# Kernel tuning notes

Measured on AMD Instinct MI355X. Metric: run time of the kernel, lower is better.

The kernel has to match this reference:

```python
import jax, jax.numpy as jnp
from jax import lax
import numpy as np

T, B, S, H = 64, 512, 10, 1024

def setup_inputs() -> dict:
    key = jax.random.key(0)
    ks = jax.random.split(key, 5)
    sc_in = 1.0 / np.sqrt(S)
    sc_h = 1.0 / np.sqrt(H)
    return {
        "inputs": jax.random.normal(ks[0], (T, B, S), jnp.float32),
        "W_in": jax.random.normal(ks[1], (S, H), jnp.float32) * sc_in,
        "b_in": jnp.zeros((H,), jnp.float32),
        "W_ih": jax.random.normal(ks[2], (4 * H, H), jnp.float32) * sc_h,
        "W_hh": jax.random.normal(ks[3], (4 * H, H), jnp.float32) * sc_h,
        "b_ih": jnp.zeros((4 * H,), jnp.float32),
        "b_hh": jnp.zeros((4 * H,), jnp.float32),
        "W_out": jax.random.normal(ks[4], (H, S), jnp.float32) * sc_h,
        "b_out": jnp.zeros((S,), jnp.float32),
    }

def reference(inputs, W_in, b_in, W_ih, W_hh, b_ih, b_hh, W_out, b_out):
    # inputs: [T, B, S]
    t, b, s = inputs.shape
    h_dim = W_hh.shape[1]
    # input Linear: S -> H, for all timesteps at once
    x = inputs @ W_in + b_in                               # [T, B, H]
    # precompute input contribution to LSTM gates (PyTorch gate order i,f,g,o)
    xg = jnp.einsum('tbh,gh->tbg', x, W_ih) + (b_ih + b_hh)  # [T, B, 4H]

    def cell(carry, xg_t):
        h, c = carry
        gates = xg_t + h @ W_hh.T                          # [B, 4H]
        i, f, g, o = jnp.split(gates, 4, axis=-1)
        i = jax.nn.sigmoid(i)
        f = jax.nn.sigmoid(f)
        g = jnp.tanh(g)
        o = jax.nn.sigmoid(o)
        c = f * c + i * g
        h = o * jnp.tanh(c)
        return (h, c), h

    h0 = jnp.zeros((b, h_dim), inputs.dtype)
    _, hs = lax.scan(cell, (h0, h0), xg)                   # hs: [T, B, H]
    out = hs @ W_out + b_out                               # [T, B, S]
    return jnp.transpose(out, (1, 0, 2))                   # [B, T, S] (stack dim=1)
```

## Files before the change

kernel.cpp:

```cpp
#include <hip/hip_runtime.h>
#include <hip/hip_bf16.h>
#include <stdint.h>

#define T_STEPS 64
#define BATCH   512
#define SDIM    10
#define HDIM    1024
#define GDIM    4096

typedef __attribute__((ext_vector_type(8))) short bf16x8;
typedef __attribute__((ext_vector_type(4))) float f32x4;

#define MFMA16(a,b,c) __builtin_amdgcn_mfma_f32_16x16x32_bf16(a,b,c,0,0,0)
#define VMW(N) asm volatile("s_waitcnt vmcnt(" #N ")" ::: "memory")
#define LGKM0  asm volatile("s_waitcnt lgkmcnt(0)" ::: "memory")
#define SBAR   do { __builtin_amdgcn_s_barrier(); __builtin_amdgcn_sched_barrier(0); } while (0)

__device__ __forceinline__ float sigmoidf_(float x) { return 1.0f / (1.0f + __expf(-x)); }
__device__ __forceinline__ float tanhf_(float x) {
    x = fminf(15.0f, fmaxf(-15.0f, x));
    float e = __expf(2.0f * x);
    return (e - 1.0f) / (e + 1.0f);
}
__device__ __forceinline__ short bf16bits(float v) {
    __hip_bfloat16 hb = __float2bfloat16(v);
    return *(short*)&hb;
}

__device__ __forceinline__ void gload16(const void* g, void* l) {
    __builtin_amdgcn_global_load_lds(
        (const __attribute__((address_space(1))) unsigned int*)g,
        (__attribute__((address_space(3))) unsigned int*)l, 16, 0, 0);
}

__global__ void setup_kernel(const float* __restrict__ W_hh,
                             const float* __restrict__ W_out,
                             __hip_bfloat16* __restrict__ whh_bf,
                             __hip_bfloat16* __restrict__ wot_bf) {
    int idx = blockIdx.x * blockDim.x + threadIdx.x;
    int stride = gridDim.x * blockDim.x;
    for (int i = idx; i < GDIM * HDIM; i += stride)
        whh_bf[i] = __float2bfloat16(W_hh[i]);
    for (int i = idx; i < 16 * HDIM; i += stride) {
        int n = i >> 10, k = i & 1023;
        wot_bf[i] = (n < SDIM) ? __float2bfloat16(W_out[k * SDIM + n]) : __float2bfloat16(0.0f);
    }
}

__launch_bounds__(256)
__global__ void weq_kernel(const float* __restrict__ W_in,
                           const float* __restrict__ W_ih,
                           const float* __restrict__ b_in,
                           const float* __restrict__ b_ih,
                           const float* __restrict__ b_hh,
                           __hip_bfloat16* __restrict__ weq_bf) {
    __shared__ float sWin[SDIM * HDIM];
    __shared__ float sbin[HDIM];
    const int tid = threadIdx.x;
    for (int i = tid; i < SDIM * HDIM; i += 256) sWin[i] = W_in[i];
    for (int i = tid; i < HDIM; i += 256) sbin[i] = b_in[i];
    __syncthreads();
    const int wv = tid >> 6, lane = tid & 63;
#pragma unroll
    for (int j = 0; j < 4; ++j) {
        int n = blockIdx.x * 16 + wv * 4 + j;
        float acc[SDIM + 1];
#pragma unroll
        for (int s = 0; s <= SDIM; s++) acc[s] = 0.0f;
        for (int it = 0; it < HDIM / 64; ++it) {
            int k = lane + it * 64;
            float wih = W_ih[n * HDIM + k];
#pragma unroll
            for (int s = 0; s < SDIM; s++) acc[s] += wih * sWin[s * HDIM + k];
            acc[SDIM] += wih * sbin[k];
        }
#pragma unroll
        for (int s = 0; s <= SDIM; s++) {
            float v = acc[s];
            for (int off = 32; off > 0; off >>= 1) v += __shfl_down(v, off);
            acc[s] = v;
        }
        if (lane == 0) {
            __hip_bfloat16 rowv[32];
#pragma unroll
            for (int s = 0; s < SDIM; s++) rowv[s] = __float2bfloat16(acc[s]);
            rowv[10] = __float2bfloat16(acc[SDIM] + b_ih[n] + b_hh[n]);
#pragma unroll
            for (int s = 11; s < 32; s++) rowv[s] = __float2bfloat16(0.0f);
#pragma unroll
            for (int q = 0; q < 4; q++)
                ((uint4*)(weq_bf + n * 32))[q] = ((uint4*)rowv)[q];
        }
    }
}

__launch_bounds__(256)
__global__ void t0_kernel(const float* __restrict__ inputs,
                          const __hip_bfloat16* __restrict__ weq_bf,
                          __hip_bfloat16* __restrict__ hs,
                          float* __restrict__ c_buf) {
    int gidx = blockIdx.x * 256 + threadIdx.x;
    int b = gidx >> 10, h = gidx & 1023;
    float xv[SDIM];
#pragma unroll
    for (int s = 0; s < SDIM; s++) xv[s] = inputs[b * SDIM + s];
    float pre[4];
#pragma unroll
    for (int g = 0; g < 4; ++g) {
        const __hip_bfloat16* wr = weq_bf + (size_t)(g * HDIM + h) * 32;
        float a = __bfloat162float(wr[10]);
#pragma unroll
        for (int s = 0; s < SDIM; s++) a += xv[s] * __bfloat162float(wr[s]);
        pre[g] = a;
    }
    float ig = sigmoidf_(pre[0]);
    float gg = tanhf_(pre[2]);
    float og = sigmoidf_(pre[3]);
    float cn = ig * gg;
    c_buf[gidx] = cn;
    hs[gidx] = __float2bfloat16(og * tanhf_(cn));
}

__launch_bounds__(256, 1)
__global__ void step_kernel(const float* __restrict__ inputs,
                            const __hip_bfloat16* __restrict__ weq_bf,
                            const __hip_bfloat16* __restrict__ whh,
                            __hip_bfloat16* __restrict__ hs,
                            float* __restrict__ c_buf,
                            int t) {
    __shared__ __align__(16) unsigned char lds[122880];
    unsigned char* augA = lds + 98304;
    unsigned char* augB = lds + 106496;

    const int tid = threadIdx.x;
    const int wv = tid >> 6, lane = tid & 63;
    const int wm = wv >> 1, wn = wv & 1;
    const int lr = lane & 15, lk = lane >> 4;

    const int bid = blockIdx.x;
    const int nb = (bid & 7) * 4 + ((bid >> 3) & 3);
    const int mb = bid >> 5;
    const int m0 = mb * 64, h0 = nb * 32;

    const __hip_bfloat16* hprev = hs + (size_t)(t - 1) * BATCH * HDIM;

    const int srow = lane >> 3, sc8 = lane & 7;
    const __hip_bfloat16* aSrc[2]; int aDst[2];
#pragma unroll
    for (int j = 0; j < 2; j++) {
        int row = wv * 16 + j * 8 + srow;
        aSrc[j] = hprev + (size_t)(m0 + row) * HDIM + ((sc8 ^ (row & 7)) << 3);
        aDst[j] = wv * 2048 + j * 1024;
    }
    const __hip_bfloat16* bSrc[4]; int bDst[4];
#pragma unroll
    for (int j = 0; j < 4; j++) {
        int c = wv * 32 + j * 8 + srow;
        int n = (c & 3) * HDIM + h0 + (c >> 2);
        bSrc[j] = whh + (size_t)n * HDIM + ((sc8 ^ (c & 7)) << 3);
        bDst[j] = 8192 + wv * 4096 + j * 1024;
    }

    auto STAGE = [&](int kt) {
        const int base = (kt & 3) * 24576;
        const int ko = kt * 64;
        gload16(aSrc[0] + ko, lds + base + aDst[0]);
        gload16(aSrc[1] + ko, lds + base + aDst[1]);
        gload16(bSrc[0] + ko, lds + base + bDst[0]);
        gload16(bSrc[1] + ko, lds + base + bDst[1]);
        gload16(bSrc[2] + ko, lds + base + bDst[2]);
        gload16(bSrc[3] + ko, lds + base + bDst[3]);
    };

    *(uint4*)(augA + tid * 32) = (uint4){0, 0, 0, 0};
    *(uint4*)(augA + tid * 32 + 16) = (uint4){0, 0, 0, 0};

    float4 xv4 = {0.f, 0.f, 0.f, 0.f};
    if (tid < 160) xv4 = *(const float4*)(inputs + (size_t)(t * BATCH + m0) * SDIM + tid * 4);
    uint4 wb[2];
#pragma unroll
    for (int i = 0; i < 2; i++) {
        int q = tid + i * 256, c = q >> 2, ch = q & 3;
        int n = (c & 3) * HDIM + h0 + (c >> 2);
        wb[i] = *(const uint4*)(weq_bf + (size_t)n * 32 + ch * 8);
    }

    STAGE(0); STAGE(1); STAGE(2);

    LGKM0; SBAR;

    if (tid < 160) {
        float xf[4] = {xv4.x, xv4.y, xv4.z, xv4.w};
#pragma unroll
        for (int q = 0; q < 4; q++) {
            int idx = tid * 4 + q, row = idx / SDIM, col = idx - row * SDIM;
            *(short*)(augA + ((row * 128 + col * 2) ^ ((row & 7) << 4))) = bf16bits(xf[q]);
        }
    }
    if (tid < 64)
        *(short*)(augA + ((tid * 128 + 20) ^ ((tid & 7) << 4))) = (short)0x3F80;
#pragma unroll
    for (int i = 0; i < 2; i++) {
        int q = tid + i * 256, c = q >> 2, ch = q & 3;
        *(uint4*)(augB + c * 128 + ((ch * 16) ^ ((c & 7) << 4))) = wb[i];
    }
    LGKM0; SBAR;

    int aro[2], asz[2], bro[4], bsz[4];
#pragma unroll
    for (int fm = 0; fm < 2; fm++) {
        int row = wm * 32 + fm * 16 + lr;
        aro[fm] = row * 128; asz[fm] = (row & 7) << 4;
    }
#pragma unroll
    for (int fn = 0; fn < 4; fn++) {
        int c = wn * 64 + fn * 16 + lr;
        bro[fn] = c * 128; bsz[fn] = (c & 7) << 4;
    }

    f32x4 acc[2][4];
#pragma unroll
    for (int fm = 0; fm < 2; fm++)
#pragma unroll
        for (int fn = 0; fn < 4; fn++) {
            f32x4 z = {0.f, 0.f, 0.f, 0.f};
            acc[fm][fn] = z;
        }
    {
        bf16x8 a[2], b[4];
#pragma unroll
        for (int fm = 0; fm < 2; fm++)
            a[fm] = *(const bf16x8*)(augA + aro[fm] + ((lk * 16) ^ asz[fm]));
#pragma unroll
        for (int fn = 0; fn < 4; fn++)
            b[fn] = *(const bf16x8*)(augB + bro[fn] + ((lk * 16) ^ bsz[fn]));
#pragma unroll
        for (int fm = 0; fm < 2; fm++)
#pragma unroll
            for (int fn = 0; fn < 4; fn++)
                acc[fm][fn] = MFMA16(a[fm], b[fn], acc[fm][fn]);
    }

    for (int i = 0; i < 16; ++i) {
        if (i < 14)      { VMW(12); }
        else if (i == 14){ VMW(6);  }
        else             { VMW(0);  }
        SBAR;
        if (i < 13) STAGE(i + 3);
        const unsigned char* Ab = lds + (i & 3) * 24576;
        const unsigned char* Bb = Ab + 8192;
#pragma unroll
        for (int ks = 0; ks < 2; ++ks) {
            const int lo = ks * 64 + lk * 16;
            bf16x8 a[2], b[4];
#pragma unroll
            for (int fm = 0; fm < 2; fm++)
                a[fm] = *(const bf16x8*)(Ab + aro[fm] + (lo ^ asz[fm]));
#pragma unroll
            for (int fn = 0; fn < 4; fn++)
                b[fn] = *(const bf16x8*)(Bb + bro[fn] + (lo ^ bsz[fn]));
#pragma unroll
            for (int fm = 0; fm < 2; fm++)
#pragma unroll
                for (int fn = 0; fn < 4; fn++)
                    acc[fm][fn] = MFMA16(a[fm], b[fn], acc[fm][fn]);
        }
    }

#pragma unroll
    for (int fm = 0; fm < 2; fm++)
#pragma unroll
        for (int fn = 0; fn < 4; fn++)
#pragma unroll
            for (int r = 0; r < 4; r++) {
                int row = wm * 32 + fm * 16 + lk * 4 + r;
                int col = wn * 64 + fn * 16 + lr;
                *(float*)(lds + ((row * 512 + col * 4) ^ ((row & 7) << 4))) = acc[fm][fn][r];
            }
    LGKM0; SBAR;

    {
        const int row = tid >> 2, hh0 = (tid & 3) * 8;
        const size_t gbase = (size_t)(m0 + row) * HDIM + h0 + hh0;
        float4 c0 = *(float4*)(c_buf + gbase);
        float4 c1 = *(float4*)(c_buf + gbase + 4);
        float cold[8] = {c0.x, c0.y, c0.z, c0.w, c1.x, c1.y, c1.z, c1.w};
        float cnew[8];
        short hv[8];
#pragma unroll
        for (int j = 0; j < 8; j++) {
            float4 g4 = *(const float4*)(lds + ((row * 512 + (hh0 + j) * 16) ^ ((row & 7) << 4)));
            float ig = sigmoidf_(g4.x);
            float fg = sigmoidf_(g4.y);
            float gg = tanhf_(g4.z);
            float og = sigmoidf_(g4.w);
            float cn = fg * cold[j] + ig * gg;
            cnew[j] = cn;
            hv[j] = bf16bits(og * tanhf_(cn));
        }
        *(float4*)(c_buf + gbase) = (float4){cnew[0], cnew[1], cnew[2], cnew[3]};
        *(float4*)(c_buf + gbase + 4) = (float4){cnew[4], cnew[5], cnew[6], cnew[7]};
        *(uint4*)(hs + (size_t)t * BATCH * HDIM + gbase) = *(uint4*)hv;
    }
}

__launch_bounds__(256)
__global__ void out_mfma(const __hip_bfloat16* __restrict__ hs,
                         const __hip_bfloat16* __restrict__ wot,
                         const float* __restrict__ b_out,
                         float* __restrict__ out) {
    __shared__ __align__(16) unsigned char sW[32768];
    const int tid = threadIdx.x, lane = tid & 63, wv = tid >> 6;
    const int lr = lane & 15, lk = lane >> 4;
#pragma unroll
    for (int i = 0; i < 8; i++) {
        int q = tid + i * 256;
        int row = q >> 7, col = q & 127;
        uint4 v = *(const uint4*)(wot + row * 1024 + col * 8);
        *(uint4*)(sW + row * 2048 + ((col * 16) ^ ((row & 7) << 4))) = v;
    }
    float bo = (lr < SDIM) ? b_out[lr] : 0.0f;
    __syncthreads();
    const int sw = (lr & 7) << 4;
    const int brow = lr * 2048;
#pragma unroll
    for (int s2 = 0; s2 < 2; s2++) {
        int strip = blockIdx.x * 8 + wv * 2 + s2;
        const __hip_bfloat16* Ab = hs + (size_t)(strip * 16 + lr) * 1024 + lk * 8;
        f32x4 acc = {0.f, 0.f, 0.f, 0.f};
        for (int kc = 0; kc < 32; kc++) {
            bf16x8 a = *(const bf16x8*)(Ab + kc * 32);
            bf16x8 b = *(const bf16x8*)(sW + brow + ((kc * 64 + lk * 16) ^ sw));
            acc = MFMA16(a, b, acc);
        }
        if (lr < SDIM) {
#pragma unroll
            for (int r = 0; r < 4; r++) {
                int grow = strip * 16 + lk * 4 + r;
                out[(grow & 511) * (T_STEPS * SDIM) + (grow >> 9) * SDIM + lr] = acc[r] + bo;
            }
        }
    }
}

extern "C" void kernel_launch(void* const* d_in, const int* in_sizes, int n_in,
                              void* d_out, int out_size, void* d_ws, size_t ws_size,
                              hipStream_t stream) {
    const float* inputs = (const float*)d_in[0];
    const float* W_in   = (const float*)d_in[1];
    const float* b_in   = (const float*)d_in[2];
    const float* W_ih   = (const float*)d_in[3];
    const float* W_hh   = (const float*)d_in[4];
    const float* b_ih   = (const float*)d_in[5];
    const float* b_hh   = (const float*)d_in[6];
    const float* W_out  = (const float*)d_in[7];
    const float* b_out  = (const float*)d_in[8];
    float* out = (float*)d_out;

    uint8_t* ws = (uint8_t*)d_ws;
    __hip_bfloat16* whh_bf = (__hip_bfloat16*)(ws);
    __hip_bfloat16* hs     = (__hip_bfloat16*)(ws + 8388608ull);
    float*          c_buf  = (float*)(ws + 75497472ull);
    __hip_bfloat16* wot_bf = (__hip_bfloat16*)(ws + 77594624ull);
    __hip_bfloat16* weq_bf = (__hip_bfloat16*)(ws + 77660160ull);

    setup_kernel<<<2048, 256, 0, stream>>>(W_hh, W_out, whh_bf, wot_bf);
    weq_kernel<<<256, 256, 0, stream>>>(W_in, W_ih, b_in, b_ih, b_hh, weq_bf);
    t0_kernel<<<2048, 256, 0, stream>>>(inputs, weq_bf, hs, c_buf);
    for (int t = 1; t < T_STEPS; t++)
        step_kernel<<<256, 256, 0, stream>>>(inputs, weq_bf, whh_bf, hs, c_buf, t);
    out_mfma<<<256, 256, 0, stream>>>(hs, wot_bf, b_out, out);
}
```

Baseline: 837.9 us.

## Use 8 waves per block with K=128 tiles and triple-buffered LDS

The recurrent step kernel now runs 512 threads (8 waves) per block instead of 256. Each wave computes a 2x2 grid of MFMA fragments rather than 2x4, so the 64x128 block tile is unchanged. The K loop moves to 128-wide tiles with a 3-stage LDS ring of 48KB stages and a 16-chunk XOR swizzle; the third stage reuses the augmented-weight region once that data has been consumed. The goal is more waves to hide memory and LDS latency and fewer loop iterations and barriers per step. The cost is more LDS per block and less register-level reuse per wave.

Result: faster. 697.8 us (-16.7%).

```diff
diff --git a/kernel.cpp b/kernel.cpp
--- a/kernel.cpp
+++ b/kernel.cpp
@@ -121,20 +121,20 @@
     hs[gidx] = __float2bfloat16(og * tanhf_(cn));
 }
 
-__launch_bounds__(256, 1)
+__launch_bounds__(512, 1)
 __global__ void step_kernel(const float* __restrict__ inputs,
                             const __hip_bfloat16* __restrict__ weq_bf,
                             const __hip_bfloat16* __restrict__ whh,
                             __hip_bfloat16* __restrict__ hs,
                             float* __restrict__ c_buf,
                             int t) {
-    __shared__ __align__(16) unsigned char lds[122880];
+    __shared__ __align__(16) unsigned char lds[147456];
     unsigned char* augA = lds + 98304;
     unsigned char* augB = lds + 106496;
 
     const int tid = threadIdx.x;
     const int wv = tid >> 6, lane = tid & 63;
-    const int wm = wv >> 1, wn = wv & 1;
+    const int wm = wv >> 2, wn = wv & 3;
     const int lr = lane & 15, lk = lane >> 4;
 
     const int bid = blockIdx.x;
@@ -144,48 +144,48 @@
 
     const __hip_bfloat16* hprev = hs + (size_t)(t - 1) * BATCH * HDIM;
 
-    const int srow = lane >> 3, sc8 = lane & 7;
-    const __hip_bfloat16* aSrc[2]; int aDst[2];
+    const int lrow = lane >> 4;
+    const int lch  = lane & 15;
+    const __hip_bfloat16* aS[2]; int aD[2];
 #pragma unroll
     for (int j = 0; j < 2; j++) {
-        int row = wv * 16 + j * 8 + srow;
-        aSrc[j] = hprev + (size_t)(m0 + row) * HDIM + ((sc8 ^ (row & 7)) << 3);
-        aDst[j] = wv * 2048 + j * 1024;
-    }
-    const __hip_bfloat16* bSrc[4]; int bDst[4];
+        int idx = wv * 2 + j;
+        int row = idx * 4 + lrow;
+        int ch  = lch ^ (row & 15);
+        aS[j] = hprev + (size_t)(m0 + row) * HDIM + ch * 8;
+        aD[j] = idx * 1024;
+    }
+    const __hip_bfloat16* bS[4]; int bD[4];
 #pragma unroll
     for (int j = 0; j < 4; j++) {
-        int c = wv * 32 + j * 8 + srow;
-        int n = (c & 3) * HDIM + h0 + (c >> 2);
-        bSrc[j] = whh + (size_t)n * HDIM + ((sc8 ^ (c & 7)) << 3);
-        bDst[j] = 8192 + wv * 4096 + j * 1024;
+        int idx = wv * 4 + j;
+        int c   = idx * 4 + lrow;
+        int n   = (c & 3) * HDIM + h0 + (c >> 2);
+        int ch  = lch ^ (c & 15);
+        bS[j] = whh + (size_t)n * HDIM + ch * 8;
+        bD[j] = 16384 + idx * 1024;
     }
 
     auto STAGE = [&](int kt) {
-        const int base = (kt & 3) * 24576;
-        const int ko = kt * 64;
-        gload16(aSrc[0] + ko, lds + base + aDst[0]);
-        gload16(aSrc[1] + ko, lds + base + aDst[1]);
-        gload16(bSrc[0] + ko, lds + base + bDst[0]);
-        gload16(bSrc[1] + ko, lds + base + bDst[1]);
-        gload16(bSrc[2] + ko, lds + base + bDst[2]);
-        gload16(bSrc[3] + ko, lds + base + bDst[3]);
+        const int base = (kt % 3) * 49152;
+        const int ko = kt * 128;
+        gload16(aS[0] + ko, lds + base + aD[0]);
+        gload16(aS[1] + ko, lds + base + aD[1]);
+        gload16(bS[0] + ko, lds + base + bD[0]);
+        gload16(bS[1] + ko, lds + base + bD[1]);
+        gload16(bS[2] + ko, lds + base + bD[2]);
+        gload16(bS[3] + ko, lds + base + bD[3]);
     };
 
-    *(uint4*)(augA + tid * 32) = (uint4){0, 0, 0, 0};
-    *(uint4*)(augA + tid * 32 + 16) = (uint4){0, 0, 0, 0};
+    *(uint4*)(augA + tid * 16) = (uint4){0, 0, 0, 0};
 
     float4 xv4 = {0.f, 0.f, 0.f, 0.f};
     if (tid < 160) xv4 = *(const float4*)(inputs + (size_t)(t * BATCH + m0) * SDIM + tid * 4);
-    uint4 wb[2];
-#pragma unroll
-    for (int i = 0; i < 2; i++) {
-        int q = tid + i * 256, c = q >> 2, ch = q & 3;
-        int n = (c & 3) * HDIM + h0 + (c >> 2);
-        wb[i] = *(const uint4*)(weq_bf + (size_t)n * 32 + ch * 8);
-    }
-
-    STAGE(0); STAGE(1); STAGE(2);
+    const int wc = tid >> 2, wch = tid & 3;
+    const int wn_idx = (wc & 3) * HDIM + h0 + (wc >> 2);
+    uint4 wb = *(const uint4*)(weq_bf + (size_t)wn_idx * 32 + wch * 8);
+
+    STAGE(0); STAGE(1);
 
     LGKM0; SBAR;
 
@@ -199,70 +199,65 @@
     }
     if (tid < 64)
         *(short*)(augA + ((tid * 128 + 20) ^ ((tid & 7) << 4))) = (short)0x3F80;
-#pragma unroll
-    for (int i = 0; i < 2; i++) {
-        int q = tid + i * 256, c = q >> 2, ch = q & 3;
-        *(uint4*)(augB + c * 128 + ((ch * 16) ^ ((c & 7) << 4))) = wb[i];
-    }
+    *(uint4*)(augB + wc * 128 + ((wch * 16) ^ ((wc & 7) << 4))) = wb;
     LGKM0; SBAR;
 
-    int aro[2], asz[2], bro[4], bsz[4];
-#pragma unroll
-    for (int fm = 0; fm < 2; fm++) {
-        int row = wm * 32 + fm * 16 + lr;
-        aro[fm] = row * 128; asz[fm] = (row & 7) << 4;
-    }
-#pragma unroll
-    for (int fn = 0; fn < 4; fn++) {
-        int c = wn * 64 + fn * 16 + lr;
-        bro[fn] = c * 128; bsz[fn] = (c & 7) << 4;
-    }
-
-    f32x4 acc[2][4];
+    int aro[2], bro[2];
+#pragma unroll
+    for (int fm = 0; fm < 2; fm++) aro[fm] = (wm * 32 + fm * 16 + lr) * 256;
+#pragma unroll
+    for (int fn = 0; fn < 2; fn++) bro[fn] = (wn * 32 + fn * 16 + lr) * 256 + 16384;
+    const int swz = lr << 4;
+
+    f32x4 acc[2][2];
 #pragma unroll
     for (int fm = 0; fm < 2; fm++)
 #pragma unroll
-        for (int fn = 0; fn < 4; fn++) {
+        for (int fn = 0; fn < 2; fn++) {
             f32x4 z = {0.f, 0.f, 0.f, 0.f};
             acc[fm][fn] = z;
         }
     {
-        bf16x8 a[2], b[4];
+        bf16x8 a[2], b[2];
+#pragma unroll
+        for (int fm = 0; fm < 2; fm++) {
+            int row = wm * 32 + fm * 16 + lr;
+            a[fm] = *(const bf16x8*)(augA + row * 128 + ((lk * 16) ^ ((row & 7) << 4)));
+        }
+#pragma unroll
+        for (int fn = 0; fn < 2; fn++) {
+            int c = wn * 32 + fn * 16 + lr;
+            b[fn] = *(const bf16x8*)(augB + c * 128 + ((lk * 16) ^ ((c & 7) << 4)));
+        }
 #pragma unroll
         for (int fm = 0; fm < 2; fm++)
-            a[fm] = *(const bf16x8*)(augA + aro[fm] + ((lk * 16) ^ asz[fm]));
-#pragma unroll
-        for (int fn = 0; fn < 4; fn++)
-            b[fn] = *(const bf16x8*)(augB + bro[fn] + ((lk * 16) ^ bsz[fn]));
-#pragma unroll
-        for (int fm = 0; fm < 2; fm++)
-#pragma unroll
-            for (int fn = 0; fn < 4; fn++)
+#pragma unroll
+            for (int fn = 0; fn < 2; fn++)
                 acc[fm][fn] = MFMA16(a[fm], b[fn], acc[fm][fn]);
     }
-
-    for (int i = 0; i < 16; ++i) {
-        if (i < 14)      { VMW(12); }
-        else if (i == 14){ VMW(6);  }
-        else             { VMW(0);  }
+    LGKM0;
+
+#pragma unroll
+    for (int i = 0; i < 8; ++i) {
+        if (i < 7) { VMW(6); } else { VMW(0); }
         SBAR;
-        if (i < 13) STAGE(i + 3);
-        const unsigned char* Ab = lds + (i & 3) * 24576;
-        const unsigned char* Bb = Ab + 8192;
-#pragma unroll
-        for (int ks = 0; ks < 2; ++ks) {
+        if (i < 6) STAGE(i + 2);
+        const unsigned char* Ab = lds + (i % 3) * 49152;
+        const unsigned char* Bb = Ab;
+#pragma unroll
+        for (int ks = 0; ks < 4; ++ks) {
             const int lo = ks * 64 + lk * 16;
-            bf16x8 a[2], b[4];
+            bf16x8 a[2], b[2];
 #pragma unroll
             for (int fm = 0; fm < 2; fm++)
-                a[fm] = *(const bf16x8*)(Ab + aro[fm] + (lo ^ asz[fm]));
-#pragma unroll
-            for (int fn = 0; fn < 4; fn++)
-                b[fn] = *(const bf16x8*)(Bb + bro[fn] + (lo ^ bsz[fn]));
+                a[fm] = *(const bf16x8*)(Ab + aro[fm] + (lo ^ swz));
+#pragma unroll
+            for (int fn = 0; fn < 2; fn++)
+                b[fn] = *(const bf16x8*)(Bb + bro[fn] + (lo ^ swz));
 #pragma unroll
             for (int fm = 0; fm < 2; fm++)
 #pragma unroll
-                for (int fn = 0; fn < 4; fn++)
+                for (int fn = 0; fn < 2; fn++)
                     acc[fm][fn] = MFMA16(a[fm], b[fn], acc[fm][fn]);
         }
     }
@@ -270,37 +265,36 @@
 #pragma unroll
     for (int fm = 0; fm < 2; fm++)
 #pragma unroll
-        for (int fn = 0; fn < 4; fn++)
+        for (int fn = 0; fn < 2; fn++)
 #pragma unroll
             for (int r = 0; r < 4; r++) {
                 int row = wm * 32 + fm * 16 + lk * 4 + r;
-                int col = wn * 64 + fn * 16 + lr;
+                int col = wn * 32 + fn * 16 + lr;
                 *(float*)(lds + ((row * 512 + col * 4) ^ ((row & 7) << 4))) = acc[fm][fn][r];
             }
     LGKM0; SBAR;
 
     {
-        const int row = tid >> 2, hh0 = (tid & 3) * 8;
-        const size_t gbase = (size_t)(m0 + row) * HDIM + h0 + hh0;
-        float4 c0 = *(float4*)(c_buf + gbase);
-        float4 c1 = *(float4*)(c_buf + gbase + 4);
-        float cold[8] = {c0.x, c0.y, c0.z, c0.w, c1.x, c1.y, c1.z, c1.w};
-        float cnew[8];
-        short hv[8];
-#pragma unroll
-        for (int j = 0; j < 8; j++) {
-            float4 g4 = *(const float4*)(lds + ((row * 512 + (hh0 + j) * 16) ^ ((row & 7) << 4)));
+        const int row = tid >> 3, hq = tid & 7;
+        const size_t gbase = (size_t)(m0 + row) * HDIM + h0 + hq * 4;
+        float4 cold = *(float4*)(c_buf + gbase);
+        float cget[4] = {cold.x, cold.y, cold.z, cold.w};
+        float cnew[4];
+        short hv[4];
+#pragma unroll
+        for (int q = 0; q < 4; q++) {
+            int hh = hq * 4 + q;
+            float4 g4 = *(const float4*)(lds + ((row * 512 + hh * 16) ^ ((row & 7) << 4)));
             float ig = sigmoidf_(g4.x);
             float fg = sigmoidf_(g4.y);
             float gg = tanhf_(g4.z);
             float og = sigmoidf_(g4.w);
-            float cn = fg * cold[j] + ig * gg;
-            cnew[j] = cn;
-            hv[j] = bf16bits(og * tanhf_(cn));
+            float cn = fg * cget[q] + ig * gg;
+            cnew[q] = cn;
+            hv[q] = bf16bits(og * tanhf_(cn));
         }
         *(float4*)(c_buf + gbase) = (float4){cnew[0], cnew[1], cnew[2], cnew[3]};
-        *(float4*)(c_buf + gbase + 4) = (float4){cnew[4], cnew[5], cnew[6], cnew[7]};
-        *(uint4*)(hs + (size_t)t * BATCH * HDIM + gbase) = *(uint4*)hv;
+        *(uint2*)(hs + (size_t)t * BATCH * HDIM + gbase) = *(uint2*)hv;
     }
 }
 
@@ -368,6 +362,6 @@
     weq_kernel<<<256, 256, 0, stream>>>(W_in, W_ih, b_in, b_ih, b_hh, weq_bf);
     t0_kernel<<<2048, 256, 0, stream>>>(inputs, weq_bf, hs, c_buf);
     for (int t = 1; t < T_STEPS; t++)
-        step_kernel<<<256, 256, 0, stream>>>(inputs, weq_bf, whh_bf, hs, c_buf, t);
+        step_kernel<<<256, 512, 0, stream>>>(inputs, weq_bf, whh_bf, hs, c_buf, t);
     out_mfma<<<256, 256, 0, stream>>>(hs, wot_bf, b_out, out);
 }
```
